# Optimization experiments

Measured on AMD Instinct MI355X. Metric: run time of the kernel, lower is better.

The kernel has to match this reference:

```python
import jax, jax.numpy as jnp
import numpy as np

N_NODES = 100000
N_GRAPHS = 256
N_EDGES = 800000


def gcn_conv(x, W, b, src, dst):
    """PyG GCNConv: self-loops + symmetric deg^-1/2 normalization + scatter-add."""
    h = x @ W  # [N, F_out]
    # degree on graph with self-loops (edge weight 1)
    deg = jax.ops.segment_sum(jnp.ones((src.shape[0],), h.dtype), dst,
                              num_segments=N_NODES) + 1.0
    dinv = jax.lax.rsqrt(deg)  # deg^-1/2, deg >= 1 so finite
    norm = dinv[src] * dinv[dst]  # [E]
    msg = h[src] * norm[:, None]  # gather + scale, [E, F_out]
    agg = jax.ops.segment_sum(msg, dst, num_segments=N_NODES)
    # self-loop contribution: dinv[i]^2 * h[i]
    agg = agg + h * (dinv * dinv)[:, None]
    return agg + b


def setup_inputs() -> dict:
    key = jax.random.key(0)
    ks = jax.random.split(key, 16)
    inp = {
        "x": jax.random.normal(ks[0], (N_NODES, 114), jnp.float32),
        "edge_index": jax.random.randint(ks[1], (2, N_EDGES), 0, N_NODES, jnp.int64)
        if jax.config.jax_enable_x64 else jax.random.randint(ks[1], (2, N_EDGES), 0, N_NODES, jnp.int32),
        "batch": jnp.sort(jax.random.randint(ks[2], (N_NODES,), 0, N_GRAPHS,
                                             jnp.int32)),
        "W1": jax.random.normal(ks[3], (114, 230), jnp.float32) * 0.09,
        "b1": jax.random.normal(ks[4], (230,), jnp.float32) * 0.01,
        "W2": jax.random.normal(ks[5], (230, 115), jnp.float32) * 0.07,
        "b2": jax.random.normal(ks[6], (115,), jnp.float32) * 0.01,
        "Wg": jax.random.normal(ks[7], (115, 64), jnp.float32) * 0.09,
        "bg": jax.random.normal(ks[8], (64,), jnp.float32) * 0.01,
        "Wf": jax.random.normal(ks[9], (64, 32), jnp.float32) * 0.12,
        "bf": jax.random.normal(ks[10], (32,), jnp.float32) * 0.01,
        "Wo": jax.random.normal(ks[11], (32, 1), jnp.float32) * 0.17,
        "bo": jax.random.normal(ks[12], (1,), jnp.float32) * 0.01,
    }
    return inp


def reference(x, edge_index, batch, W1, b1, W2, b2, Wg, bg, Wf, bf, Wo, bo):
    src, dst = edge_index[0], edge_index[1]
    h = jax.nn.relu(gcn_conv(x, W1, b1, src, dst))
    # dropout p=0.2 is identity at inference (training=False)
    h = jax.nn.relu(gcn_conv(h, W2, b2, src, dst))
    # global max pool over graphs; h >= 0 after relu so clamp empty segments to 0
    pooled = jax.ops.segment_max(h, batch, num_segments=N_GRAPHS)
    pooled = jnp.maximum(pooled, 0.0)  # [G, 115]
    g = jax.nn.relu(pooled @ Wg + bg)
    g = jax.nn.relu(g @ Wf + bf)
    return g @ Wo + bo  # [G, 1]
```

## Files before the change

### kernel.cpp

```cpp
#include <hip/hip_runtime.h>
#include <hip/hip_bf16.h>
#include <hip/hip_fp16.h>

#define NN 100000
#define NG 256
#define NE 800000

constexpr int F0 = 114;
constexpr int F1 = 230;
constexpr int F2 = 115;
constexpr int MPAD = 100096;

typedef _Float16 __attribute__((ext_vector_type(8))) f16x8;
typedef __attribute__((ext_vector_type(4))) float f32x4;
typedef __attribute__((ext_vector_type(8))) unsigned short u16x8;

__device__ __forceinline__ unsigned short f2h_bits(float x) {
  _Float16 h = (_Float16)x;
  return __builtin_bit_cast(unsigned short, h);
}
__device__ __forceinline__ float h_bits2f(unsigned short u) {
  return (float)__builtin_bit_cast(_Float16, u);
}

__device__ __forceinline__ void bar_nodrain() {
  asm volatile("s_waitcnt lgkmcnt(0)" ::: "memory");
  __builtin_amdgcn_s_barrier();
}


__global__ void k_count(const int* __restrict__ dst, int* __restrict__ cnt) {
  int e = blockIdx.x * blockDim.x + threadIdx.x;
  if (e < NE) atomicAdd(&cnt[dst[e]], 1);
}

constexpr int SCAN_T = 256;
constexpr int SCAN_E = 1024;
constexpr int NB = (NN + SCAN_E - 1) / SCAN_E;

__global__ void k_scan1(const int* __restrict__ cnt, int* __restrict__ off,
                        int* __restrict__ bsum, float* __restrict__ dinv) {
  __shared__ int s[SCAN_T];
  int b = blockIdx.x, t = threadIdx.x;
  int base = b * SCAN_E + t * 4;
  int v0 = 0, v1 = 0, v2 = 0, v3 = 0;
  if (base + 0 < NN) v0 = cnt[base + 0];
  if (base + 1 < NN) v1 = cnt[base + 1];
  if (base + 2 < NN) v2 = cnt[base + 2];
  if (base + 3 < NN) v3 = cnt[base + 3];
  if (base + 0 < NN) dinv[base + 0] = rsqrtf((float)v0 + 1.0f);
  if (base + 1 < NN) dinv[base + 1] = rsqrtf((float)v1 + 1.0f);
  if (base + 2 < NN) dinv[base + 2] = rsqrtf((float)v2 + 1.0f);
  if (base + 3 < NN) dinv[base + 3] = rsqrtf((float)v3 + 1.0f);
  int sum = v0 + v1 + v2 + v3;
  s[t] = sum;
  __syncthreads();
  for (int ofs = 1; ofs < SCAN_T; ofs <<= 1) {
    int x = (t >= ofs) ? s[t - ofs] : 0;
    __syncthreads();
    s[t] += x;
    __syncthreads();
  }
  int excl = s[t] - sum;
  if (base + 0 < NN) off[base + 0] = excl;
  if (base + 1 < NN) off[base + 1] = excl + v0;
  if (base + 2 < NN) off[base + 2] = excl + v0 + v1;
  if (base + 3 < NN) off[base + 3] = excl + v0 + v1 + v2;
  if (t == SCAN_T - 1) bsum[b] = s[t];
}

__global__ void k_scan3(int* __restrict__ off, const int* __restrict__ bsum,
                        int* __restrict__ cur) {
  __shared__ int pre;
  int b = blockIdx.x, t = threadIdx.x;
  int seg = b >> 2;
  if (t < 64) {
    int s = 0;
    for (int j = t; j < seg; j += 64) s += bsum[j];
#pragma unroll
    for (int o = 1; o < 64; o <<= 1) s += __shfl_xor(s, o);
    if (t == 0) pre = s;
  }
  __syncthreads();
  int i = b * 256 + t;
  if (i < NN) {
    int v = off[i] + pre;
    off[i] = v;
    cur[i] = v;
  }
  if (i == NN) off[NN] = NE;
}


constexpr int FB_PLACE = (NE + 255) / 256;
constexpr int FB_PREPX = NN / 2;
constexpr int FB_PREPB = 256;
constexpr int FB_POOL  = (NG * F2 + 255) / 256;

__global__ __launch_bounds__(256) void k_fatB(
    const int* __restrict__ src, const int* __restrict__ dst,
    int* __restrict__ cur, int* __restrict__ srcs,
    const float* __restrict__ x, const float* __restrict__ dinv,
    unsigned short* __restrict__ xd,
    const float* __restrict__ W1, const float* __restrict__ W2,
    unsigned short* __restrict__ B1h, unsigned short* __restrict__ B1l,
    unsigned short* __restrict__ B2h, unsigned short* __restrict__ B2l,
    float* __restrict__ pooled) {
  int b = blockIdx.x, t = threadIdx.x;
  if (b < FB_PLACE) {
    int e = b * 256 + t;
    if (e < NE) {
      int p = atomicAdd(&cur[dst[e]], 1);
      srcs[p] = src[e];
    }
  } else if (b < FB_PLACE + FB_PREPX) {
    int bb = b - FB_PLACE;
    int n = bb * 2 + (t >> 7);
    int f = t & 127;
    float v = (f < F0) ? x[(size_t)n * F0 + f] * dinv[n] : 0.0f;
    xd[(size_t)n * 128 + f] = f2h_bits(v);
  } else if (b < FB_PLACE + FB_PREPX + FB_PREPB) {
    int bb = b - (FB_PLACE + FB_PREPX);
    if (bb < 128) {
      int n = bb * 2 + (t >> 7), k = t & 127;
      float v = (k < F0 && n < F1) ? W1[(size_t)k * F1 + n] : 0.0f;
      unsigned short h = f2h_bits(v);
      unsigned short l = f2h_bits(v - h_bits2f(h));
      B1h[(size_t)n * 128 + k] = h;
      B1l[(size_t)n * 128 + k] = l;
    } else {
      int n = bb - 128, k = t;
      float v = (k < F1 && n < F2) ? W2[(size_t)k * F2 + n] : 0.0f;
      unsigned short h = f2h_bits(v);
      unsigned short l = f2h_bits(v - h_bits2f(h));
      B2h[(size_t)n * 256 + k] = h;
      B2l[(size_t)n * 256 + k] = l;
    }
  } else {
    int bb = b - (FB_PLACE + FB_PREPX + FB_PREPB);
    int i = bb * 256 + t;
    if (i < NG * F2) pooled[i] = 0.0f;
  }
}


template <bool POOL>
__global__ __launch_bounds__(256) void k_gatherw(
    const unsigned short* __restrict__ tab, const float* __restrict__ dinv,
    const int* __restrict__ off, const int* __restrict__ srcs,
    const float* __restrict__ b2, const int* __restrict__ batch,
    unsigned short* __restrict__ outh, float* __restrict__ pooled) {
  __shared__ float smax[4][128];
  __shared__ int sg[4];
  int w = threadIdx.x >> 6, lane = threadIdx.x & 63;
  int n = blockIdx.x * 4 + w;
  int grp = lane >> 4, sub = lane & 15;
  int fb = sub * 8;

  float acc[8] = {0.f, 0.f, 0.f, 0.f, 0.f, 0.f, 0.f, 0.f};
  int j0 = off[n], j1 = off[n + 1];
  for (int base = j0; base <= j1; base += 16) {
    int row[4];
    u16x8 v[4];
    bool has[4];
#pragma unroll
    for (int c = 0; c < 4; ++c) {
      int je = base + c * 4 + grp;
      row[c] = (je < j1) ? srcs[je] : ((je == j1) ? n : -1);
      has[c] = row[c] >= 0;
    }
#pragma unroll
    for (int c = 0; c < 4; ++c)
      if (has[c]) v[c] = *(const u16x8*)&tab[(size_t)row[c] * 128 + fb];
#pragma unroll
    for (int c = 0; c < 4; ++c)
      if (has[c]) {
#pragma unroll
        for (int u = 0; u < 8; ++u) acc[u] += h_bits2f(v[c][u]);
      }
  }
#pragma unroll
  for (int u = 0; u < 8; ++u) {
    acc[u] += __shfl_xor(acc[u], 16);
    acc[u] += __shfl_xor(acc[u], 32);
  }
  float dn = dinv[n];

  if constexpr (!POOL) {
    if (grp == 0) {
      u16x8 o;
#pragma unroll
      for (int u = 0; u < 8; ++u) o[u] = f2h_bits(acc[u] * dn);
      *(u16x8*)&outh[(size_t)n * 128 + fb] = o;
    }
  } else {
    if (grp == 0) {
#pragma unroll
      for (int u = 0; u < 8; ++u) {
        int f = fb + u;
        float bb = (f < F2) ? b2[f] : 0.0f;
        smax[w][f] = fmaxf(acc[u] * dn + bb, 0.0f);
      }
      if (sub == 0) sg[w] = batch[n];
    }
    __syncthreads();
    int t = threadIdx.x;
    if (t < 128) {
      int g0 = sg[0];
      bool same = (sg[1] == g0) & (sg[2] == g0) & (sg[3] == g0);
      if (same) {
        float m = fmaxf(fmaxf(smax[0][t], smax[1][t]),
                        fmaxf(smax[2][t], smax[3][t]));
        if (t < F2 && m > 0.0f)
          atomicMax((int*)&pooled[g0 * F2 + t], __float_as_int(m));
      } else {
        for (int ww = 0; ww < 4; ++ww) {
          float m = smax[ww][t];
          if (t < F2 && m > 0.0f)
            atomicMax((int*)&pooled[sg[ww] * F2 + t], __float_as_int(m));
        }
      }
    }
  }
}


__global__ __launch_bounds__(256) void k_fused(
    const unsigned short* __restrict__ A,
    const unsigned short* __restrict__ B1h, const unsigned short* __restrict__ B1l,
    const unsigned short* __restrict__ B2h, const unsigned short* __restrict__ B2l,
    const float* __restrict__ b1, const float* __restrict__ dscale,
    unsigned short* __restrict__ td) {
  __shared__ char lds[81920];
  char* h1B = lds;
  char* AsB = lds + 32768;
  char* Bs0 = lds + 49152;
  char* Bs1 = lds + 65536;

  const int t = threadIdx.x;
  const int m0 = blockIdx.x * 64;
  const int lane = t & 63, w = t >> 6;
  const int r = lane & 15;
  const int kq = lane >> 4;
  const int kb16 = kq * 16;
  const int rq = kq * 4;
  const int wc = w * 32;
  const int swr = (r & 7) << 4;
  const int arow = t >> 2, aseg = t & 3, aswz = (arow & 7) << 4;
  const int brow = t >> 1, bseg = t & 1, bswz = (brow & 7) << 4;

  {
    size_t ga = (size_t)(m0 + arow) * 128 + aseg * 32;
#pragma unroll
    for (int v = 0; v < 4; ++v) {
      u16x8 d = *(const u16x8*)&A[ga + v * 8];
      *(u16x8*)(AsB + arow * 256 + ((aseg * 64 + v * 16) ^ aswz)) = d;
    }
  }
  u16x8 ph[4], pl[4];
  {
    size_t gb = (size_t)brow * 128 + bseg * 32;
#pragma unroll
    for (int v = 0; v < 4; ++v) {
      ph[v] = *(const u16x8*)&B1h[gb + v * 8];
      pl[v] = *(const u16x8*)&B1l[gb + v * 8];
    }
  }

  f32x4 acc1[4][2], acc2[4][2];
#pragma unroll
  for (int i = 0; i < 4; ++i)
#pragma unroll
    for (int j = 0; j < 2; ++j) {
      acc1[i][j] = (f32x4){0.f, 0.f, 0.f, 0.f};
      acc2[i][j] = (f32x4){0.f, 0.f, 0.f, 0.f};
    }

#pragma unroll
  for (int rd = 0; rd < 8; ++rd) {
    bar_nodrain();
#pragma unroll
    for (int v = 0; v < 4; ++v) {
      const int bo = (bseg * 64 + v * 16) ^ bswz;
      *(u16x8*)(Bs0 + brow * 128 + bo) = ph[v];
      *(u16x8*)(Bs1 + brow * 128 + bo) = pl[v];
    }
    if (rd < 7) {
      const int nr = rd + 1;
      const unsigned short* Gh = (nr < 4) ? B1h : B2h;
      const unsigned short* Gl = (nr < 4) ? B1l : B2l;
      const size_t gb = (nr < 4)
          ? (size_t)((nr >> 1) * 128 + brow) * 128 + (nr & 1) * 64 + bseg * 32
          : (size_t)brow * 256 + (nr - 4) * 64 + bseg * 32;
#pragma unroll
      for (int v = 0; v < 4; ++v) {
        ph[v] = *(const u16x8*)&Gh[gb + v * 8];
        pl[v] = *(const u16x8*)&Gl[gb + v * 8];
      }
    }
    bar_nodrain();

    if (rd < 4) {
      const int kc = rd & 1;
#pragma unroll
      for (int ks = 0; ks < 2; ++ks) {
        f16x8 av[4], bh[2], bl[2];
#pragma unroll
        for (int i = 0; i < 4; ++i)
          av[i] = *(const f16x8*)(AsB + (i * 16 + r) * 256 +
                                  ((kc * 128 + ks * 64 + kb16) ^ swr));
#pragma unroll
        for (int j = 0; j < 2; ++j) {
          const int row = wc + j * 16 + r;
          const int bo = (ks * 64 + kb16) ^ swr;
          bh[j] = *(const f16x8*)(Bs0 + row * 128 + bo);
          bl[j] = *(const f16x8*)(Bs1 + row * 128 + bo);
        }
        __builtin_amdgcn_s_setprio(1);
#pragma unroll
        for (int i = 0; i < 4; ++i)
#pragma unroll
          for (int j = 0; j < 2; ++j)
            acc1[i][j] = __builtin_amdgcn_mfma_f32_16x16x32_f16(av[i], bl[j], acc1[i][j], 0, 0, 0);
#pragma unroll
        for (int i = 0; i < 4; ++i)
#pragma unroll
          for (int j = 0; j < 2; ++j)
            acc1[i][j] = __builtin_amdgcn_mfma_f32_16x16x32_f16(av[i], bh[j], acc1[i][j], 0, 0, 0);
        __builtin_amdgcn_s_setprio(0);
      }
      if (rd == 1 || rd == 3) {
        const int h = rd >> 1;
#pragma unroll
        for (int i = 0; i < 4; ++i)
#pragma unroll
          for (int j = 0; j < 2; ++j) {
            const int nl = wc + j * 16 + r;
            const int n = h * 128 + nl;
            const bool val = n < F1;
            const float bb = val ? b1[n] : 0.0f;
#pragma unroll
            for (int q = 0; q < 4; ++q) {
              const int ml = i * 16 + rq + q;
              const float v = val ? fmaxf(acc1[i][j][q] + bb, 0.0f) : 0.0f;
              *(unsigned short*)(h1B + ml * 512 + ((n * 2) ^ ((ml & 7) << 4))) = f2h_bits(v);
            }
          }
#pragma unroll
        for (int i = 0; i < 4; ++i)
#pragma unroll
          for (int j = 0; j < 2; ++j) acc1[i][j] = (f32x4){0.f, 0.f, 0.f, 0.f};
      }
    } else {
      const int kc = rd - 4;
#pragma unroll
      for (int ks = 0; ks < 2; ++ks) {
        f16x8 ah[4], bh[2], bl[2];
#pragma unroll
        for (int i = 0; i < 4; ++i) {
          const int row = i * 16 + r;
          ah[i] = *(const f16x8*)(h1B + row * 512 + ((kc * 128 + ks * 64 + kb16) ^ swr));
        }
#pragma unroll
        for (int j = 0; j < 2; ++j) {
          const int row = wc + j * 16 + r;
          const int bo = (ks * 64 + kb16) ^ swr;
          bh[j] = *(const f16x8*)(Bs0 + row * 128 + bo);
          bl[j] = *(const f16x8*)(Bs1 + row * 128 + bo);
        }
        __builtin_amdgcn_s_setprio(1);
#pragma unroll
        for (int i = 0; i < 4; ++i)
#pragma unroll
          for (int j = 0; j < 2; ++j)
            acc2[i][j] = __builtin_amdgcn_mfma_f32_16x16x32_f16(ah[i], bl[j], acc2[i][j], 0, 0, 0);
#pragma unroll
        for (int i = 0; i < 4; ++i)
#pragma unroll
          for (int j = 0; j < 2; ++j)
            acc2[i][j] = __builtin_amdgcn_mfma_f32_16x16x32_f16(ah[i], bh[j], acc2[i][j], 0, 0, 0);
        __builtin_amdgcn_s_setprio(0);
      }
    }
  }

  __syncthreads();
#pragma unroll
  for (int i = 0; i < 4; ++i)
#pragma unroll
    for (int j = 0; j < 2; ++j) {
      const int nl = wc + j * 16 + r;
#pragma unroll
      for (int q = 0; q < 4; ++q) {
        const int ml = i * 16 + rq + q;
        const float v = acc2[i][j][q] * dscale[m0 + ml];
        *(unsigned short*)(h1B + ml * 512 + ((nl * 2) ^ ((ml & 7) << 4))) = f2h_bits(v);
      }
    }
  __syncthreads();
  {
    const int row = t >> 2, seg = t & 3;
    const int swz = (row & 7) << 4;
    const size_t dst = (size_t)(m0 + row) * 128 + seg * 32;
#pragma unroll
    for (int v = 0; v < 4; ++v) {
      u16x8 d = *(const u16x8*)(h1B + row * 512 + ((seg * 64 + v * 16) ^ swz));
      *(u16x8*)&td[dst + v * 8] = d;
    }
  }
}


__global__ void k_mlp(const float* __restrict__ pooled,
                      const float* __restrict__ Wg, const float* __restrict__ bg,
                      const float* __restrict__ Wf, const float* __restrict__ bf,
                      const float* __restrict__ Wo, const float* __restrict__ bo,
                      float* __restrict__ out) {
  __shared__ float sp[F2];
  __shared__ float sg[64];
  __shared__ float sf[32];
  int g = blockIdx.x, t = threadIdx.x;
  for (int f = t; f < F2; f += 64) sp[f] = pooled[g * F2 + f];
  __syncthreads();
  float a = bg[t];
  for (int k = 0; k < F2; ++k) a += sp[k] * Wg[k * 64 + t];
  sg[t] = fmaxf(a, 0.0f);
  __syncthreads();
  if (t < 32) {
    float c = bf[t];
    for (int k = 0; k < 64; ++k) c += sg[k] * Wf[k * 32 + t];
    sf[t] = fmaxf(c, 0.0f);
  }
  __syncthreads();
  if (t == 0) {
    float c = bo[0];
    for (int k = 0; k < 32; ++k) c += sf[k] * Wo[k];
    out[g] = c;
  }
}


extern "C" void kernel_launch(void* const* d_in, const int* in_sizes, int n_in,
                              void* d_out, int out_size, void* d_ws, size_t ws_size,
                              hipStream_t stream) {
  const float* x  = (const float*)d_in[0];
  const int* ei   = (const int*)d_in[1];
  const int* batch = (const int*)d_in[2];
  const float* W1 = (const float*)d_in[3];
  const float* b1 = (const float*)d_in[4];
  const float* W2 = (const float*)d_in[5];
  const float* b2 = (const float*)d_in[6];
  const float* Wg = (const float*)d_in[7];
  const float* bg = (const float*)d_in[8];
  const float* Wf = (const float*)d_in[9];
  const float* bf = (const float*)d_in[10];
  const float* Wo = (const float*)d_in[11];
  const float* bo = (const float*)d_in[12];
  const int* src = ei;
  const int* dst = ei + NE;

  char* p = (char*)d_ws;
  auto alloc4 = [&](size_t units) { void* r = p; p += units * 4; return r; };
  float* dinv  = (float*)alloc4(100224);
  int* cnt     = (int*)alloc4(100224);
  int* off     = (int*)alloc4(100352);
  int* cur     = (int*)alloc4(100224);
  int* bsum    = (int*)alloc4(128);
  int* srcs    = (int*)alloc4(NE);
  unsigned short* xd   = (unsigned short*)alloc4((size_t)NN * 128 / 2);
  unsigned short* aggX = (unsigned short*)alloc4((size_t)MPAD * 128 / 2);
  unsigned short* td   = (unsigned short*)alloc4((size_t)MPAD * 128 / 2);
  unsigned short* Bt1h = (unsigned short*)alloc4(256 * 128 / 2);
  unsigned short* Bt1l = (unsigned short*)alloc4(256 * 128 / 2);
  unsigned short* Bt2h = (unsigned short*)alloc4(128 * 256 / 2);
  unsigned short* Bt2l = (unsigned short*)alloc4(128 * 256 / 2);
  float* pooled = (float*)alloc4((size_t)NG * F2);

  hipMemsetAsync(cnt, 0, 100224 * sizeof(int), stream);

  k_count<<<(NE + 255) / 256, 256, 0, stream>>>(dst, cnt);
  k_scan1<<<NB, SCAN_T, 0, stream>>>(cnt, off, bsum, dinv);
  k_scan3<<<(NN + 256) / 256, 256, 0, stream>>>(off, bsum, cur);

  k_fatB<<<FB_PLACE + FB_PREPX + FB_PREPB + FB_POOL, 256, 0, stream>>>(
      src, dst, cur, srcs, x, dinv, xd, W1, W2,
      Bt1h, Bt1l, Bt2h, Bt2l, pooled);

  k_gatherw<false><<<NN / 4, 256, 0, stream>>>(xd, dinv, off, srcs,
                                               nullptr, nullptr, aggX, nullptr);

  k_fused<<<MPAD / 64, 256, 0, stream>>>(aggX, Bt1h, Bt1l, Bt2h, Bt2l,
                                         b1, dinv, td);

  k_gatherw<true><<<NN / 4, 256, 0, stream>>>(td, dinv, off, srcs,
                                              b2, batch, nullptr, pooled);

  k_mlp<<<NG, 64, 0, stream>>>(pooled, Wg, bg, Wf, bf, Wo, bo, (float*)d_out);
}
```

Baseline: 291.8 us.

## Drop fp16 hi/lo weight split and restructure fused GEMM to cut LDS

Weights are now converted to a single fp16 copy instead of a hi/lo pair, so the fused two-layer GEMM issues half as many MFMAs and loads half the B data. The intermediate h1 tile is reorganized so the layer-2 accumulation interleaves with per-half layer-1 outputs, shrinking shared memory from 80KB to 48KB and adding launch bounds for 3 blocks per CU. This trades weight precision (fp16 rounding error in W1/W2) for fewer instructions and higher occupancy. The restructured loop order (h, phase, kc) changes how layer-2 consumes h1 and must be checked for correctness.

```diff
diff --git a/kernel.cpp b/kernel.cpp
--- a/kernel.cpp
+++ b/kernel.cpp
@@ -103,8 +103,7 @@
     const float* __restrict__ x, const float* __restrict__ dinv,
     unsigned short* __restrict__ xd,
     const float* __restrict__ W1, const float* __restrict__ W2,
-    unsigned short* __restrict__ B1h, unsigned short* __restrict__ B1l,
-    unsigned short* __restrict__ B2h, unsigned short* __restrict__ B2l,
+    unsigned short* __restrict__ B1, unsigned short* __restrict__ B2,
     float* __restrict__ pooled) {
   int b = blockIdx.x, t = threadIdx.x;
   if (b < FB_PLACE) {
@@ -124,17 +123,11 @@
     if (bb < 128) {
       int n = bb * 2 + (t >> 7), k = t & 127;
       float v = (k < F0 && n < F1) ? W1[(size_t)k * F1 + n] : 0.0f;
-      unsigned short h = f2h_bits(v);
-      unsigned short l = f2h_bits(v - h_bits2f(h));
-      B1h[(size_t)n * 128 + k] = h;
-      B1l[(size_t)n * 128 + k] = l;
+      B1[(size_t)n * 128 + k] = f2h_bits(v);
     } else {
       int n = bb - 128, k = t;
       float v = (k < F1 && n < F2) ? W2[(size_t)k * F2 + n] : 0.0f;
-      unsigned short h = f2h_bits(v);
-      unsigned short l = f2h_bits(v - h_bits2f(h));
-      B2h[(size_t)n * 256 + k] = h;
-      B2l[(size_t)n * 256 + k] = l;
+      B2[(size_t)n * 256 + k] = f2h_bits(v);
     }
   } else {
     int bb = b - (FB_PLACE + FB_PREPX + FB_PREPB);
@@ -225,17 +218,16 @@
 }
 
 
-__global__ __launch_bounds__(256) void k_fused(
+__global__ __launch_bounds__(256, 3) void k_fused(
     const unsigned short* __restrict__ A,
-    const unsigned short* __restrict__ B1h, const unsigned short* __restrict__ B1l,
-    const unsigned short* __restrict__ B2h, const unsigned short* __restrict__ B2l,
+    const unsigned short* __restrict__ B1,
+    const unsigned short* __restrict__ B2,
     const float* __restrict__ b1, const float* __restrict__ dscale,
     unsigned short* __restrict__ td) {
-  __shared__ char lds[81920];
-  char* h1B = lds;
-  char* AsB = lds + 32768;
-  char* Bs0 = lds + 49152;
-  char* Bs1 = lds + 65536;
+  __shared__ char lds[49152];
+  char* AsB = lds;
+  char* h1B = lds + 16384;
+  char* Bs  = lds + 32768;
 
   const int t = threadIdx.x;
   const int m0 = blockIdx.x * 64;
@@ -257,14 +249,11 @@
       *(u16x8*)(AsB + arow * 256 + ((aseg * 64 + v * 16) ^ aswz)) = d;
     }
   }
-  u16x8 ph[4], pl[4];
+  u16x8 ph[4];
   {
     size_t gb = (size_t)brow * 128 + bseg * 32;
 #pragma unroll
-    for (int v = 0; v < 4; ++v) {
-      ph[v] = *(const u16x8*)&B1h[gb + v * 8];
-      pl[v] = *(const u16x8*)&B1l[gb + v * 8];
-    }
+    for (int v = 0; v < 4; ++v) ph[v] = *(const u16x8*)&B1[gb + v * 8];
   }
 
   f32x4 acc1[4][2], acc2[4][2];
@@ -278,59 +267,41 @@
 
 #pragma unroll
   for (int rd = 0; rd < 8; ++rd) {
+    const int h = rd >> 2, phase = (rd >> 1) & 1, kc = rd & 1;
     bar_nodrain();
 #pragma unroll
-    for (int v = 0; v < 4; ++v) {
-      const int bo = (bseg * 64 + v * 16) ^ bswz;
-      *(u16x8*)(Bs0 + brow * 128 + bo) = ph[v];
-      *(u16x8*)(Bs1 + brow * 128 + bo) = pl[v];
-    }
+    for (int v = 0; v < 4; ++v)
+      *(u16x8*)(Bs + brow * 128 + ((bseg * 64 + v * 16) ^ bswz)) = ph[v];
     if (rd < 7) {
-      const int nr = rd + 1;
-      const unsigned short* Gh = (nr < 4) ? B1h : B2h;
-      const unsigned short* Gl = (nr < 4) ? B1l : B2l;
-      const size_t gb = (nr < 4)
-          ? (size_t)((nr >> 1) * 128 + brow) * 128 + (nr & 1) * 64 + bseg * 32
-          : (size_t)brow * 256 + (nr - 4) * 64 + bseg * 32;
-#pragma unroll
-      for (int v = 0; v < 4; ++v) {
-        ph[v] = *(const u16x8*)&Gh[gb + v * 8];
-        pl[v] = *(const u16x8*)&Gl[gb + v * 8];
-      }
+      const int nr = rd + 1, nh = nr >> 2, nph = (nr >> 1) & 1, nkc = nr & 1;
+      const unsigned short* G = (nph == 0) ? B1 : B2;
+      const size_t gb = (nph == 0)
+          ? (size_t)(nh * 128 + brow) * 128 + nkc * 64 + bseg * 32
+          : (size_t)brow * 256 + nh * 128 + nkc * 64 + bseg * 32;
+#pragma unroll
+      for (int v = 0; v < 4; ++v) ph[v] = *(const u16x8*)&G[gb + v * 8];
     }
     bar_nodrain();
 
-    if (rd < 4) {
-      const int kc = rd & 1;
+    if (phase == 0) {
 #pragma unroll
       for (int ks = 0; ks < 2; ++ks) {
-        f16x8 av[4], bh[2], bl[2];
+        f16x8 av[4], bv[2];
 #pragma unroll
         for (int i = 0; i < 4; ++i)
           av[i] = *(const f16x8*)(AsB + (i * 16 + r) * 256 +
                                   ((kc * 128 + ks * 64 + kb16) ^ swr));
 #pragma unroll
-        for (int j = 0; j < 2; ++j) {
-          const int row = wc + j * 16 + r;
-          const int bo = (ks * 64 + kb16) ^ swr;
-          bh[j] = *(const f16x8*)(Bs0 + row * 128 + bo);
-          bl[j] = *(const f16x8*)(Bs1 + row * 128 + bo);
-        }
-        __builtin_amdgcn_s_setprio(1);
+        for (int j = 0; j < 2; ++j)
+          bv[j] = *(const f16x8*)(Bs + (wc + j * 16 + r) * 128 +
+                                  ((ks * 64 + kb16) ^ swr));
 #pragma unroll
         for (int i = 0; i < 4; ++i)
 #pragma unroll
           for (int j = 0; j < 2; ++j)
-            acc1[i][j] = __builtin_amdgcn_mfma_f32_16x16x32_f16(av[i], bl[j], acc1[i][j], 0, 0, 0);
-#pragma unroll
-        for (int i = 0; i < 4; ++i)
-#pragma unroll
-          for (int j = 0; j < 2; ++j)
-            acc1[i][j] = __builtin_amdgcn_mfma_f32_16x16x32_f16(av[i], bh[j], acc1[i][j], 0, 0, 0);
-        __builtin_amdgcn_s_setprio(0);
-      }
-      if (rd == 1 || rd == 3) {
-        const int h = rd >> 1;
+            acc1[i][j] = __builtin_amdgcn_mfma_f32_16x16x32_f16(av[i], bv[j], acc1[i][j], 0, 0, 0);
+      }
+      if (kc == 1) {
 #pragma unroll
         for (int i = 0; i < 4; ++i)
 #pragma unroll
@@ -343,7 +314,7 @@
             for (int q = 0; q < 4; ++q) {
               const int ml = i * 16 + rq + q;
               const float v = val ? fmaxf(acc1[i][j][q] + bb, 0.0f) : 0.0f;
-              *(unsigned short*)(h1B + ml * 512 + ((n * 2) ^ ((ml & 7) << 4))) = f2h_bits(v);
+              *(unsigned short*)(h1B + ml * 256 + ((nl * 2) ^ ((ml & 7) << 4))) = f2h_bits(v);
             }
           }
 #pragma unroll
@@ -352,34 +323,24 @@
           for (int j = 0; j < 2; ++j) acc1[i][j] = (f32x4){0.f, 0.f, 0.f, 0.f};
       }
     } else {
-      const int kc = rd - 4;
 #pragma unroll
       for (int ks = 0; ks < 2; ++ks) {
-        f16x8 ah[4], bh[2], bl[2];
+        f16x8 ah[4], bv[2];
 #pragma unroll
         for (int i = 0; i < 4; ++i) {
           const int row = i * 16 + r;
-          ah[i] = *(const f16x8*)(h1B + row * 512 + ((kc * 128 + ks * 64 + kb16) ^ swr));
+          ah[i] = *(const f16x8*)(h1B + row * 256 +
+                                  ((kc * 128 + ks * 64 + kb16) ^ swr));
         }
 #pragma unroll
-        for (int j = 0; j < 2; ++j) {
-          const int row = wc + j * 16 + r;
-          const int bo = (ks * 64 + kb16) ^ swr;
-          bh[j] = *(const f16x8*)(Bs0 + row * 128 + bo);
-          bl[j] = *(const f16x8*)(Bs1 + row * 128 + bo);
-        }
-        __builtin_amdgcn_s_setprio(1);
+        for (int j = 0; j < 2; ++j)
+          bv[j] = *(const f16x8*)(Bs + (wc + j * 16 + r) * 128 +
+                                  ((ks * 64 + kb16) ^ swr));
 #pragma unroll
         for (int i = 0; i < 4; ++i)
 #pragma unroll
           for (int j = 0; j < 2; ++j)
-            acc2[i][j] = __builtin_amdgcn_mfma_f32_16x16x32_f16(ah[i], bl[j], acc2[i][j], 0, 0, 0);
-#pragma unroll
-        for (int i = 0; i < 4; ++i)
-#pragma unroll
-          for (int j = 0; j < 2; ++j)
-            acc2[i][j] = __builtin_amdgcn_mfma_f32_16x16x32_f16(ah[i], bh[j], acc2[i][j], 0, 0, 0);
-        __builtin_amdgcn_s_setprio(0);
+            acc2[i][j] = __builtin_amdgcn_mfma_f32_16x16x32_f16(ah[i], bv[j], acc2[i][j], 0, 0, 0);
       }
     }
   }
@@ -394,7 +355,7 @@
       for (int q = 0; q < 4; ++q) {
         const int ml = i * 16 + rq + q;
         const float v = acc2[i][j][q] * dscale[m0 + ml];
-        *(unsigned short*)(h1B + ml * 512 + ((nl * 2) ^ ((ml & 7) << 4))) = f2h_bits(v);
+        *(unsigned short*)(h1B + ml * 256 + ((nl * 2) ^ ((ml & 7) << 4))) = f2h_bits(v);
       }
     }
   __syncthreads();
@@ -404,7 +365,7 @@
     const size_t dst = (size_t)(m0 + row) * 128 + seg * 32;
 #pragma unroll
     for (int v = 0; v < 4; ++v) {
-      u16x8 d = *(const u16x8*)(h1B + row * 512 + ((seg * 64 + v * 16) ^ swz));
+      u16x8 d = *(const u16x8*)(h1B + row * 256 + ((seg * 64 + v * 16) ^ swz));
       *(u16x8*)&td[dst + v * 8] = d;
     }
   }
@@ -470,10 +431,8 @@
   unsigned short* xd   = (unsigned short*)alloc4((size_t)NN * 128 / 2);
   unsigned short* aggX = (unsigned short*)alloc4((size_t)MPAD * 128 / 2);
   unsigned short* td   = (unsigned short*)alloc4((size_t)MPAD * 128 / 2);
-  unsigned short* Bt1h = (unsigned short*)alloc4(256 * 128 / 2);
-  unsigned short* Bt1l = (unsigned short*)alloc4(256 * 128 / 2);
-  unsigned short* Bt2h = (unsigned short*)alloc4(128 * 256 / 2);
-  unsigned short* Bt2l = (unsigned short*)alloc4(128 * 256 / 2);
+  unsigned short* Bt1  = (unsigned short*)alloc4(256 * 128 / 2);
+  unsigned short* Bt2  = (unsigned short*)alloc4(128 * 256 / 2);
   float* pooled = (float*)alloc4((size_t)NG * F2);
 
   hipMemsetAsync(cnt, 0, 100224 * sizeof(int), stream);
@@ -483,14 +442,12 @@
   k_scan3<<<(NN + 256) / 256, 256, 0, stream>>>(off, bsum, cur);
 
   k_fatB<<<FB_PLACE + FB_PREPX + FB_PREPB + FB_POOL, 256, 0, stream>>>(
-      src, dst, cur, srcs, x, dinv, xd, W1, W2,
-      Bt1h, Bt1l, Bt2h, Bt2l, pooled);
+      src, dst, cur, srcs, x, dinv, xd, W1, W2, Bt1, Bt2, pooled);
 
   k_gatherw<false><<<NN / 4, 256, 0, stream>>>(xd, dinv, off, srcs,
                                                nullptr, nullptr, aggX, nullptr);
 
-  k_fused<<<MPAD / 64, 256, 0, stream>>>(aggX, Bt1h, Bt1l, Bt2h, Bt2l,
-                                         b1, dinv, td);
+  k_fused<<<MPAD / 64, 256, 0, stream>>>(aggX, Bt1, Bt2, b1, dinv, td);
 
   k_gatherw<true><<<NN / 4, 256, 0, stream>>>(td, dinv, off, srcs,
                                               b2, batch, nullptr, pooled);
```

Measured after the change: 272.0 us, median of 2. 1.07x faster.
